# Performance work log

Hardware: AMD Instinct MI355X
Metric: run time of the kernel (lower is better)

The kernel has to match this reference:

```python
import jax, jax.numpy as jnp
import numpy as np

N = 524288          # batch == input_size (original code feeds the (N,) ndi vector straight into Linear(input_size,10))
K = 66              # knots: torch.linspace(0, 1, 66)
_xk = np.linspace(0.0, 1.0, K).astype(np.float32)
_dx = np.diff(_xk).astype(np.float32)  # (K-1,), uniform h = 1/65


def _notaknot_matrix():
    # scipy.interpolate.CubicSpline default bc_type='not-a-knot': solve A @ s = b for the
    # first derivatives s at the knots. Interior rows are the standard tridiagonal C2 conditions;
    # first/last rows enforce continuity of the third derivative (not-a-knot).
    A = np.zeros((K, K), np.float32)
    dx = _dx
    i = np.arange(1, K - 1)
    A[i, i - 1] = dx[1:]
    A[i, i] = 2.0 * (dx[1:] + dx[:-1])
    A[i, i + 1] = dx[:-1]
    A[0, 0] = dx[1]
    A[0, 1] = _xk[2] - _xk[0]
    A[-1, -1] = dx[-2]
    A[-1, -2] = _xk[-1] - _xk[-3]
    return A

_A = _notaknot_matrix()


def _fit(y):
    # y: (N, K). Returns per-interval secant slopes (N, K-1) and knot derivatives s (N, K).
    dx = jnp.asarray(_dx)
    slope = (y[:, 1:] - y[:, :-1]) / dx
    d02 = float(_xk[2] - _xk[0])
    dl = float(_xk[-1] - _xk[-3])
    dx0 = float(_dx[0]); dx1 = float(_dx[1]); dxm1 = float(_dx[-1]); dxm2 = float(_dx[-2])
    b0 = ((dx0 + 2.0 * d02) * dx1 * slope[:, 0] + dx0 * dx0 * slope[:, 1]) / d02
    bl = (dxm1 * dxm1 * slope[:, -2] + (2.0 * dl + dxm1) * dxm2 * slope[:, -1]) / dl
    bi = 3.0 * (dx[1:] * slope[:, :-1] + dx[:-1] * slope[:, 1:])  # (N, K-2)
    b = jnp.concatenate([b0[:, None], bi, bl[:, None]], axis=1)   # (N, K)
    s = jnp.linalg.solve(jnp.asarray(_A), b.T).T                  # factor A once, N RHS
    return slope, s


def _eval(y, slope, s, t):
    # Evaluate every row's spline at scalar t (Hermite form, matches scipy coefficients).
    xk = jnp.asarray(_xk)
    k = jnp.clip(jnp.searchsorted(xk, t, side='right') - 1, 0, K - 2)
    h = xk[k + 1] - xk[k]
    u = t - xk[k]
    sk = s[:, k]
    sk1 = s[:, k + 1]
    mk = slope[:, k]
    tt = (sk + sk1 - 2.0 * mk) / h
    c0 = tt / h
    c1 = (mk - sk) / h - tt
    return ((c0 * u + c1) * u + sk) * u + y[:, k]


def setup_inputs() -> dict:
    key = jax.random.key(0)
    ks = jax.random.split(key, 6)
    x = jax.random.uniform(ks[0], (N, K), jnp.float32)
    soc = jax.random.uniform(ks[1], (N,), jnp.float32)
    lim1 = float(1.0 / np.sqrt(N))
    W1 = jax.random.uniform(ks[2], (10, N), jnp.float32, -lim1, lim1)
    b1 = jax.random.uniform(ks[3], (10,), jnp.float32, -lim1, lim1)
    lim2 = float(1.0 / np.sqrt(10.0))
    W2 = jax.random.uniform(ks[4], (1, 10), jnp.float32, -lim2, lim2)
    b2 = jax.random.uniform(ks[5], (1,), jnp.float32, -lim2, lim2)
    return {"x": x, "soc": soc, "i": jnp.asarray(0.1, jnp.float32), "j": jnp.asarray(0.9, jnp.float32),
            "W1": W1, "b1": b1, "W2": W2, "b2": b2}


def reference(x, soc, i, j, W1, b1, W2, b2):
    slope, s = _fit(x)
    r_i = _eval(x, slope, s, i)   # (N,)
    r_j = _eval(x, slope, s, j)   # (N,)
    ndis = (r_i - r_j) / (r_i + r_j)           # (N,)
    h1 = W1 @ ndis + b1                        # (10,)  -- original feeds 1-D ndis into Linear
    h1 = jnp.where(h1 > 0, h1, 0.01 * h1)      # LeakyReLU(0.01)
    soc_hat = W2 @ h1 + b2                     # (1,)
    loss = jnp.sum((soc_hat - soc) ** 2)       # MSELoss(reduction='sum') with broadcasting
    return soc_hat, ndis, loss
```

## Files before the change

### kernel.cpp

```cpp
#include <hip/hip_runtime.h>

#define NROW 524288
#define KDIM 66
#define NSEG 65
#define NB   2048
#define PART_STRIDE 12

#define WOFF_P 528

struct Pre {
    float  xk[KDIM];
    float  dxf[NSEG];
    double av[KDIM];
    double winv[KDIM];
    double cp[KDIM];
    double dxinv[NSEG];
    double d3[NSEG];
    double pp, qq, r1, r2;
};

constexpr Pre make_pre() {
    Pre p{};
    for (int k = 0; k < KDIM; ++k) p.xk[k] = (float)((1.0 / 65.0) * (double)k);
    p.xk[KDIM - 1] = 1.0f;
    for (int k = 0; k < NSEG; ++k) p.dxf[k] = p.xk[k + 1] - p.xk[k];

    double d02 = (double)(p.xk[2] - p.xk[0]);
    double dl  = (double)(p.xk[KDIM - 1] - p.xk[KDIM - 3]);

    double bv[KDIM] = {};
    double cv[KDIM] = {};
    bv[0] = (double)p.dxf[1];
    bv[KDIM - 1] = (double)p.dxf[KDIM - 3];
    for (int i = 1; i < KDIM - 1; ++i)
        bv[i] = 2.0 * ((double)p.dxf[i] + (double)p.dxf[i - 1]);
    p.av[0] = 0.0;
    p.av[1] = d02;
    for (int i = 2; i < KDIM; ++i) p.av[i] = (double)p.dxf[i - 2];
    for (int i = 0; i < KDIM - 2; ++i) cv[i] = (double)p.dxf[i + 1];
    cv[KDIM - 2] = dl;
    cv[KDIM - 1] = 0.0;

    double w = bv[0];
    p.winv[0] = 1.0 / w;
    p.cp[0]   = cv[0] / w;
    for (int i = 1; i < KDIM; ++i) {
        w = bv[i] - p.av[i] * p.cp[i - 1];
        p.winv[i] = 1.0 / w;
        p.cp[i]   = cv[i] / w;
    }
    for (int m = 0; m < NSEG; ++m) {
        p.dxinv[m] = 1.0 / (double)p.dxf[m];
        p.d3[m]    = 3.0 * (double)p.dxf[m];
    }
    p.pp = ((double)p.dxf[0] + 2.0 * d02) * (double)p.dxf[1] / d02;
    p.qq = (double)p.dxf[0] * (double)p.dxf[0] / d02;
    p.r1 = (double)p.dxf[64] * (double)p.dxf[64] / dl;
    p.r2 = (2.0 * dl + (double)p.dxf[64]) * (double)p.dxf[63] / dl;
    return p;
}

__device__ constexpr Pre PRE = make_pre();

__global__ __launch_bounds__(64) void setup_kernel(const float* __restrict__ ti,
                                                   const float* __restrict__ tj,
                                                   float* __restrict__ wout) {
    __shared__ double dp_s[2][KDIM];
    __shared__ double z_s[2][KDIM];
    const int tid = threadIdx.x;
    if (tid >= 2) return;
    const float t = (tid == 0) ? ti[0] : tj[0];
    float* wo = wout + tid * KDIM;

    int kk = 0;
    float xkk = PRE.xk[0], xkk1 = PRE.xk[1];
#pragma unroll
    for (int k = 0; k <= KDIM - 2; ++k) {
        if (PRE.xk[k] <= t) { kk = k; xkk = PRE.xk[k]; xkk1 = PRE.xk[k + 1]; }
    }

    const double h  = (double)(xkk1 - xkk);
    const double u  = (double)(t - xkk);
    const double u2 = u * u, u3 = u2 * u, h2 = h * h;
    const double alpha = u3 / h2 - 2.0 * u2 / h + u;
    const double beta  = u3 / h2 - u2 / h;
    const double gamma = 3.0 * u2 / h - 2.0 * u3 / h2;

    double dpv = 0.0;
#pragma unroll
    for (int i = 0; i < KDIM; ++i) {
        double rhs = (i == kk) ? alpha : ((i == kk + 1) ? beta : 0.0);
        dpv = (rhs - PRE.av[i] * dpv) * PRE.winv[i];
        dp_s[tid][i] = dpv;
    }

    double zv = dp_s[tid][KDIM - 1];
    z_s[tid][KDIM - 1] = zv;
#pragma unroll
    for (int i = KDIM - 2; i >= 0; --i) {
        zv = dp_s[tid][i] - PRE.cp[i] * zv;
        z_s[tid][i] = zv;
    }

    const double z0  = z_s[tid][0];
    const double z65 = z_s[tid][KDIM - 1];
    double c = z0 * PRE.pp;
    double carryW = 0.0;
#pragma unroll
    for (int j = 1; j <= 64; ++j) {
        const double zj = z_s[tid][j];
        double full = c + zj * PRE.d3[j];
        if (j - 1 == kk) full += gamma;
        if (j == 64)     full += z65 * PRE.r1;
        const double w = full * PRE.dxinv[j - 1];
        double wy = carryW - w;
        if (j - 1 == kk) wy += 1.0;
        wo[j - 1] = (float)wy;
        carryW = w;
        c = zj * PRE.d3[j - 1];
        if (j == 1) c += z0 * PRE.qq;
    }
    double full64 = c + z65 * PRE.r2;
    if (kk == 64) full64 += gamma;
    const double w64 = full64 * PRE.dxinv[64];
    double wy64 = carryW - w64;
    if (kk == 64) wy64 += 1.0;
    wo[64] = (float)wy64;
    wo[65] = (float)w64;
}

__global__ __launch_bounds__(256) void main_kernel(
    const float* __restrict__ x, const float* __restrict__ soc,
    const float* __restrict__ W1, const float* __restrict__ wglob,
    float* __restrict__ out_ndis, double* __restrict__ partials)
{
    __shared__ __align__(16) float wi_s[KDIM];
    __shared__ __align__(16) float wj_s[KDIM];
    __shared__ double red[4][12];
    const int tid = threadIdx.x;

    if (tid < KDIM)            wi_s[tid]        = wglob[tid];
    else if (tid < 2 * KDIM)   wj_s[tid - KDIM] = wglob[tid];
    __syncthreads();

    const int n = blockIdx.x * 256 + tid;

    float w1v[10];
#pragma unroll
    for (int o = 0; o < 10; ++o) w1v[o] = W1[(size_t)o * NROW + n];
    const float socv = soc[n];

    const float2* __restrict__ row = (const float2*)(x + (size_t)n * KDIM);
    const float2* wi2 = (const float2*)wi_s;
    const float2* wj2 = (const float2*)wj_s;
    float ri = 0.f, rj = 0.f;
#pragma unroll
    for (int k = 0; k < KDIM / 2; ++k) {
        const float2 v = row[k];
        const float2 a = wi2[k];
        const float2 b = wj2[k];
        ri = fmaf(v.x, a.x, ri); ri = fmaf(v.y, a.y, ri);
        rj = fmaf(v.x, b.x, rj); rj = fmaf(v.y, b.y, rj);
    }

    const float nd = (ri - rj) / (ri + rj);
    out_ndis[n] = nd;

    const double ndd = (double)nd;
    double acc[12];
#pragma unroll
    for (int o = 0; o < 10; ++o) acc[o] = (double)w1v[o] * ndd;
    const double sv = (double)socv;
    acc[10] = sv;
    acc[11] = sv * sv;

#pragma unroll
    for (int o = 0; o < 12; ++o) {
        double v = acc[o];
#pragma unroll
        for (int off = 32; off > 0; off >>= 1) v += __shfl_down(v, off, 64);
        acc[o] = v;
    }
    const int wid  = tid >> 6;
    const int lane = tid & 63;
    if (lane == 0) {
#pragma unroll
        for (int o = 0; o < 12; ++o) red[wid][o] = acc[o];
    }
    __syncthreads();
    if (tid < 12) {
        double s = red[0][tid] + red[1][tid] + red[2][tid] + red[3][tid];
        partials[(size_t)blockIdx.x * PART_STRIDE + tid] = s;
    }
}

__global__ void finalize_kernel(const double* __restrict__ partials,
                                const float* __restrict__ b1,
                                const float* __restrict__ W2,
                                const float* __restrict__ b2,
                                float* __restrict__ out)
{
    __shared__ double red[16][16];
    __shared__ double totals[12];
    int tid = threadIdx.x;
    int o = tid & 15, g = tid >> 4;
    double s = 0.0;
    if (o < 12) {
        for (int b = g; b < NB; b += 16)
            s += partials[(size_t)b * PART_STRIDE + o];
    }
    red[g][o] = s;
    __syncthreads();
    if (tid < 12) {
        double tot = 0.0;
        for (int g2 = 0; g2 < 16; ++g2) tot += red[g2][tid];
        totals[tid] = tot;
    }
    __syncthreads();
    if (tid == 0) {
        double acc = 0.0;
#pragma unroll
        for (int o2 = 0; o2 < 10; ++o2) {
            double h1 = totals[o2] + (double)b1[o2];
            h1 = (h1 > 0.0) ? h1 : 0.01 * h1;
            acc += (double)W2[o2] * h1;
        }
        double shat = acc + (double)b2[0];
        out[0] = (float)shat;
        double ssum = totals[10], ssum2 = totals[11];
        double loss = (double)NROW * shat * shat - 2.0 * shat * ssum + ssum2;
        out[1 + NROW] = (float)loss;
    }
}

extern "C" void kernel_launch(void* const* d_in, const int* in_sizes, int n_in,
                              void* d_out, int out_size, void* d_ws, size_t ws_size,
                              hipStream_t stream) {
    const float* x   = (const float*)d_in[0];
    const float* soc = (const float*)d_in[1];
    const float* ti  = (const float*)d_in[2];
    const float* tj  = (const float*)d_in[3];
    const float* W1  = (const float*)d_in[4];
    const float* b1  = (const float*)d_in[5];
    const float* W2  = (const float*)d_in[6];
    const float* b2  = (const float*)d_in[7];
    float* out = (float*)d_out;

    float*  wglob    = (float*)d_ws;
    double* partials = (double*)((char*)d_ws + WOFF_P);

    setup_kernel<<<1, 64, 0, stream>>>(ti, tj, wglob);
    main_kernel<<<NB, 256, 0, stream>>>(x, soc, W1, wglob, out + 1, partials);
    finalize_kernel<<<1, 256, 0, stream>>>(partials, b1, W2, b2, out);
}
```

Baseline: 278.7 us.

## Fuse setup, main and finalize kernels into one with last-block reduction

Merges the spline-weight setup, the per-row evaluation and the final reduction into a single kernel. Every block now recomputes the interpolation weights for both evaluation points into shared memory. The last block to finish, found through an atomic counter, reduces the partials and writes the scalar outputs. This removes two kernel launches and their inter-kernel gaps, but adds a memset launch and a serial double-precision setup step at the start of every block.

New measurement: 633.2 us. +127.2%, slower.

```diff
diff --git a/kernel.cpp b/kernel.cpp
--- a/kernel.cpp
+++ b/kernel.cpp
@@ -6,7 +6,7 @@
 #define NB   2048
 #define PART_STRIDE 12
 
-#define WOFF_P 528
+#define CNT_OFF (NB * PART_STRIDE * 8)
 
 struct Pre {
     float  xk[KDIM];
@@ -62,85 +62,86 @@
 
 __device__ constexpr Pre PRE = make_pre();
 
-__global__ __launch_bounds__(64) void setup_kernel(const float* __restrict__ ti,
-                                                   const float* __restrict__ tj,
-                                                   float* __restrict__ wout) {
-    __shared__ double dp_s[2][KDIM];
-    __shared__ double z_s[2][KDIM];
-    const int tid = threadIdx.x;
-    if (tid >= 2) return;
-    const float t = (tid == 0) ? ti[0] : tj[0];
-    float* wo = wout + tid * KDIM;
-
-    int kk = 0;
-    float xkk = PRE.xk[0], xkk1 = PRE.xk[1];
-#pragma unroll
-    for (int k = 0; k <= KDIM - 2; ++k) {
-        if (PRE.xk[k] <= t) { kk = k; xkk = PRE.xk[k]; xkk1 = PRE.xk[k + 1]; }
-    }
-
-    const double h  = (double)(xkk1 - xkk);
-    const double u  = (double)(t - xkk);
-    const double u2 = u * u, u3 = u2 * u, h2 = h * h;
-    const double alpha = u3 / h2 - 2.0 * u2 / h + u;
-    const double beta  = u3 / h2 - u2 / h;
-    const double gamma = 3.0 * u2 / h - 2.0 * u3 / h2;
-
-    double dpv = 0.0;
-#pragma unroll
-    for (int i = 0; i < KDIM; ++i) {
-        double rhs = (i == kk) ? alpha : ((i == kk + 1) ? beta : 0.0);
-        dpv = (rhs - PRE.av[i] * dpv) * PRE.winv[i];
-        dp_s[tid][i] = dpv;
-    }
-
-    double zv = dp_s[tid][KDIM - 1];
-    z_s[tid][KDIM - 1] = zv;
-#pragma unroll
-    for (int i = KDIM - 2; i >= 0; --i) {
-        zv = dp_s[tid][i] - PRE.cp[i] * zv;
-        z_s[tid][i] = zv;
-    }
-
-    const double z0  = z_s[tid][0];
-    const double z65 = z_s[tid][KDIM - 1];
-    double c = z0 * PRE.pp;
-    double carryW = 0.0;
-#pragma unroll
-    for (int j = 1; j <= 64; ++j) {
-        const double zj = z_s[tid][j];
-        double full = c + zj * PRE.d3[j];
-        if (j - 1 == kk) full += gamma;
-        if (j == 64)     full += z65 * PRE.r1;
-        const double w = full * PRE.dxinv[j - 1];
-        double wy = carryW - w;
-        if (j - 1 == kk) wy += 1.0;
-        wo[j - 1] = (float)wy;
-        carryW = w;
-        c = zj * PRE.d3[j - 1];
-        if (j == 1) c += z0 * PRE.qq;
-    }
-    double full64 = c + z65 * PRE.r2;
-    if (kk == 64) full64 += gamma;
-    const double w64 = full64 * PRE.dxinv[64];
-    double wy64 = carryW - w64;
-    if (kk == 64) wy64 += 1.0;
-    wo[64] = (float)wy64;
-    wo[65] = (float)w64;
-}
-
-__global__ __launch_bounds__(256) void main_kernel(
+__global__ __launch_bounds__(256) void fused_kernel(
     const float* __restrict__ x, const float* __restrict__ soc,
-    const float* __restrict__ W1, const float* __restrict__ wglob,
-    float* __restrict__ out_ndis, double* __restrict__ partials)
+    const float* __restrict__ W1,
+    const float* __restrict__ ti, const float* __restrict__ tj,
+    const float* __restrict__ b1, const float* __restrict__ W2,
+    const float* __restrict__ b2,
+    float* __restrict__ out, double* __restrict__ partials,
+    unsigned int* __restrict__ counter)
 {
     __shared__ __align__(16) float wi_s[KDIM];
     __shared__ __align__(16) float wj_s[KDIM];
+    __shared__ double dp_s[2][KDIM];
+    __shared__ double z_s[2][KDIM];
     __shared__ double red[4][12];
+    __shared__ double red2[16][16];
+    __shared__ double totals[12];
+    __shared__ unsigned int is_last;
+
     const int tid = threadIdx.x;
 
-    if (tid < KDIM)            wi_s[tid]        = wglob[tid];
-    else if (tid < 2 * KDIM)   wj_s[tid - KDIM] = wglob[tid];
+    if (tid < 2) {
+        const float t = (tid == 0) ? ti[0] : tj[0];
+        float* wo = (tid == 0) ? wi_s : wj_s;
+
+        int kk = 0;
+        float xkk = PRE.xk[0], xkk1 = PRE.xk[1];
+#pragma unroll
+        for (int k = 0; k <= KDIM - 2; ++k) {
+            if (PRE.xk[k] <= t) { kk = k; xkk = PRE.xk[k]; xkk1 = PRE.xk[k + 1]; }
+        }
+
+        const double h  = (double)(xkk1 - xkk);
+        const double u  = (double)(t - xkk);
+        const double u2 = u * u, u3 = u2 * u, h2 = h * h;
+        const double alpha = u3 / h2 - 2.0 * u2 / h + u;
+        const double beta  = u3 / h2 - u2 / h;
+        const double gamma = 3.0 * u2 / h - 2.0 * u3 / h2;
+
+        double dpv = 0.0;
+#pragma unroll
+        for (int i = 0; i < KDIM; ++i) {
+            double rhs = (i == kk) ? alpha : ((i == kk + 1) ? beta : 0.0);
+            dpv = (rhs - PRE.av[i] * dpv) * PRE.winv[i];
+            dp_s[tid][i] = dpv;
+        }
+
+        double zv = dp_s[tid][KDIM - 1];
+        z_s[tid][KDIM - 1] = zv;
+#pragma unroll
+        for (int i = KDIM - 2; i >= 0; --i) {
+            zv = dp_s[tid][i] - PRE.cp[i] * zv;
+            z_s[tid][i] = zv;
+        }
+
+        const double z0  = z_s[tid][0];
+        const double z65 = z_s[tid][KDIM - 1];
+        double c = z0 * PRE.pp;
+        double carryW = 0.0;
+#pragma unroll
+        for (int j = 1; j <= 64; ++j) {
+            const double zj = z_s[tid][j];
+            double full = c + zj * PRE.d3[j];
+            if (j - 1 == kk) full += gamma;
+            if (j == 64)     full += z65 * PRE.r1;
+            const double w = full * PRE.dxinv[j - 1];
+            double wy = carryW - w;
+            if (j - 1 == kk) wy += 1.0;
+            wo[j - 1] = (float)wy;
+            carryW = w;
+            c = zj * PRE.d3[j - 1];
+            if (j == 1) c += z0 * PRE.qq;
+        }
+        double full64 = c + z65 * PRE.r2;
+        if (kk == 64) full64 += gamma;
+        const double w64 = full64 * PRE.dxinv[64];
+        double wy64 = carryW - w64;
+        if (kk == 64) wy64 += 1.0;
+        wo[64] = (float)wy64;
+        wo[65] = (float)w64;
+    }
     __syncthreads();
 
     const int n = blockIdx.x * 256 + tid;
@@ -164,7 +165,7 @@
     }
 
     const float nd = (ri - rj) / (ri + rj);
-    out_ndis[n] = nd;
+    out[1 + n] = nd;
 
     const double ndd = (double)nd;
     double acc[12];
@@ -192,44 +193,44 @@
         double s = red[0][tid] + red[1][tid] + red[2][tid] + red[3][tid];
         partials[(size_t)blockIdx.x * PART_STRIDE + tid] = s;
     }
-}
-
-__global__ void finalize_kernel(const double* __restrict__ partials,
-                                const float* __restrict__ b1,
-                                const float* __restrict__ W2,
-                                const float* __restrict__ b2,
-                                float* __restrict__ out)
-{
-    __shared__ double red[16][16];
-    __shared__ double totals[12];
-    int tid = threadIdx.x;
-    int o = tid & 15, g = tid >> 4;
-    double s = 0.0;
-    if (o < 12) {
-        for (int b = g; b < NB; b += 16)
-            s += partials[(size_t)b * PART_STRIDE + o];
-    }
-    red[g][o] = s;
-    __syncthreads();
-    if (tid < 12) {
-        double tot = 0.0;
-        for (int g2 = 0; g2 < 16; ++g2) tot += red[g2][tid];
-        totals[tid] = tot;
-    }
+
+    __threadfence();
     __syncthreads();
     if (tid == 0) {
-        double acc = 0.0;
-#pragma unroll
-        for (int o2 = 0; o2 < 10; ++o2) {
-            double h1 = totals[o2] + (double)b1[o2];
-            h1 = (h1 > 0.0) ? h1 : 0.01 * h1;
-            acc += (double)W2[o2] * h1;
-        }
-        double shat = acc + (double)b2[0];
-        out[0] = (float)shat;
-        double ssum = totals[10], ssum2 = totals[11];
-        double loss = (double)NROW * shat * shat - 2.0 * shat * ssum + ssum2;
-        out[1 + NROW] = (float)loss;
+        unsigned int old = atomicAdd(counter, 1u);
+        is_last = (old == NB - 1) ? 1u : 0u;
+    }
+    __syncthreads();
+    if (is_last) {
+        __threadfence();
+        const int o = tid & 15, g = tid >> 4;
+        double s = 0.0;
+        if (o < 12) {
+            for (int b = g; b < NB; b += 16)
+                s += partials[(size_t)b * PART_STRIDE + o];
+        }
+        red2[g][o] = s;
+        __syncthreads();
+        if (tid < 12) {
+            double tot = 0.0;
+            for (int g2 = 0; g2 < 16; ++g2) tot += red2[g2][tid];
+            totals[tid] = tot;
+        }
+        __syncthreads();
+        if (tid == 0) {
+            double a2 = 0.0;
+#pragma unroll
+            for (int o2 = 0; o2 < 10; ++o2) {
+                double h1 = totals[o2] + (double)b1[o2];
+                h1 = (h1 > 0.0) ? h1 : 0.01 * h1;
+                a2 += (double)W2[o2] * h1;
+            }
+            double shat = a2 + (double)b2[0];
+            out[0] = (float)shat;
+            double ssum = totals[10], ssum2 = totals[11];
+            double loss = (double)NROW * shat * shat - 2.0 * shat * ssum + ssum2;
+            out[1 + NROW] = (float)loss;
+        }
     }
 }
 
@@ -246,10 +247,10 @@
     const float* b2  = (const float*)d_in[7];
     float* out = (float*)d_out;
 
-    float*  wglob    = (float*)d_ws;
-    double* partials = (double*)((char*)d_ws + WOFF_P);
-
-    setup_kernel<<<1, 64, 0, stream>>>(ti, tj, wglob);
-    main_kernel<<<NB, 256, 0, stream>>>(x, soc, W1, wglob, out + 1, partials);
-    finalize_kernel<<<1, 256, 0, stream>>>(partials, b1, W2, b2, out);
+    double*       partials = (double*)d_ws;
+    unsigned int* counter  = (unsigned int*)((char*)d_ws + CNT_OFF);
+
+    hipMemsetAsync(counter, 0, sizeof(unsigned int), stream);
+    fused_kernel<<<NB, 256, 0, stream>>>(x, soc, W1, ti, tj, b1, W2, b2,
+                                         out, partials, counter);
 }
```
